# Kernel tuning notes

Measured on AMD Instinct MI355X. Metric: run time of the kernel, lower is better.

## Reference

```python
import jax, jax.numpy as jnp
import numpy as np

SEQ = 2048
HIDDEN = 2048
INPUT = 2048
THETA = 3
TRUNC = 128  # truncated-BPTT length (divides SEQ)


def setup_inputs() -> dict:
    key = jax.random.key(0)
    k0, k1, k2, k3, k4 = jax.random.split(key, 5)
    inp = jax.random.normal(k0, (1, SEQ, INPUT), jnp.float32)
    internal = jax.random.normal(k1, (THETA + 1, SEQ, HIDDEN), jnp.float32) * 0.1
    state = jax.random.normal(k2, (1, 1, HIDDEN), jnp.float32) * 0.1
    weight_ih = jax.random.normal(k3, (HIDDEN, INPUT), jnp.float32) / np.sqrt(INPUT).astype(np.float32)
    weight_hh = jax.random.normal(k4, (HIDDEN, HIDDEN), jnp.float32) * np.float32(0.5 / np.sqrt(HIDDEN))
    bias = jnp.zeros((HIDDEN,), jnp.float32)
    return {"input": inp, "internal": internal, "state": state,
            "weight_ih": weight_ih, "weight_hh": weight_hh, "bias": bias,
            "theta": THETA}


def reference(input, internal, state, weight_ih, weight_hh, bias, theta):
    theta = int(theta)
    seq = input.shape[1]
    hidden = weight_hh.shape[0]
    # pad input along theta dim to theta+1 (torch: F.pad with zeros at the end of dim 0)
    x = jnp.pad(input, ((0, theta + 1 - input.shape[0]), (0, 0), (0, 0)))
    # Precompute the input-driven part of the cell for every (theta, t):
    # cell: h' = relu(x @ Wih^T + internal + bias + h @ Whh^T)
    pre = jnp.einsum('tsi,hi->tsh', x, weight_ih) + internal + bias  # [theta+1, seq, hidden]
    n_chunks = seq // TRUNC
    # [n_chunks, TRUNC, theta+1, hidden]
    pre_c = pre.transpose(1, 0, 2).reshape(n_chunks, TRUNC, theta + 1, hidden)

    def cell(p, h):
        return jax.nn.relu(p + h @ weight_hh.T)

    def step(h, pre_t):  # pre_t: [theta+1, hidden]
        h0 = cell(pre_t[0], h)
        outs = [h0]
        hth = h0
        for th in range(1, theta + 1):
            hth = cell(pre_t[th], hth)
            outs.append(hth)
        # continuousTheta=False: carry state from the base (th=0) step
        return h0, jnp.stack(outs, 0)  # [theta+1, hidden]

    def chunk(h, pre_chunk):
        h, outs = jax.lax.scan(step, h, pre_chunk)
        # truncated BPTT: detach state between chunks (identity in fwd)
        return jax.lax.stop_gradient(h), outs

    h0 = state[0, 0]  # [hidden]
    h_final, outs = jax.lax.scan(chunk, h0, pre_c)
    # outs: [n_chunks, TRUNC, theta+1, hidden] -> [theta+1, seq, hidden]
    outputs = outs.reshape(seq, theta + 1, hidden).transpose(1, 0, 2)
    return outputs, h_final[None, None, :]
```

## Files before the change

### kernel.cpp

```cpp
#include <hip/hip_runtime.h>
#include <stdint.h>

#define SEQ 2048
#define HID 2048
#define INP 2048
#define NTH 4

typedef uint32_t u32x4 __attribute__((ext_vector_type(4)));

template<int CTRL>
__device__ __forceinline__ float dpp_add(float x) {
    int y = __builtin_amdgcn_update_dpp(0, __float_as_int(x), CTRL, 0xF, 0xF, true);
    return x + __int_as_float(y);
}
__device__ __forceinline__ float wave_sum64(float x) {
    x = dpp_add<0x111>(x);
    x = dpp_add<0x112>(x);
    x = dpp_add<0x114>(x);
    x = dpp_add<0x118>(x);
    x = dpp_add<0x142>(x);
    x = dpp_add<0x143>(x);
    return x;
}

template<int RELU>
__global__ __launch_bounds__(256, 2)
void gemm_abt(const float* __restrict__ A, const float* __restrict__ B,
              const float* __restrict__ D, const float* __restrict__ bias,
              float* __restrict__ C, int M, int N, int K) {
    __shared__ float sA[16][132];
    __shared__ float sB[16][68];
    const int tid = threadIdx.x;
    const int tx  = tid & 15;
    const int ty  = tid >> 4;
    const int m0  = blockIdx.y * 128;
    const int n0  = blockIdx.x * 64;

    float acc[8][4];
#pragma unroll
    for (int i = 0; i < 8; ++i)
#pragma unroll
        for (int j = 0; j < 4; ++j) acc[i][j] = 0.f;

    const int srow = tid >> 2;
    const int skq  = (tid & 3) * 4;

    for (int kt = 0; kt < K; kt += 16) {
#pragma unroll
        for (int s = 0; s < 2; ++s) {
            const int row = srow + s * 64;
            float4 va = *reinterpret_cast<const float4*>(&A[(size_t)(m0 + row) * K + kt + skq]);
            sA[skq + 0][row] = va.x; sA[skq + 1][row] = va.y;
            sA[skq + 2][row] = va.z; sA[skq + 3][row] = va.w;
        }
        {
            float4 vb = *reinterpret_cast<const float4*>(&B[(size_t)(n0 + srow) * K + kt + skq]);
            sB[skq + 0][srow] = vb.x; sB[skq + 1][srow] = vb.y;
            sB[skq + 2][srow] = vb.z; sB[skq + 3][srow] = vb.w;
        }
        __syncthreads();
#pragma unroll
        for (int k = 0; k < 16; ++k) {
            float a[8], b[4];
            *reinterpret_cast<float4*>(&a[0]) = *reinterpret_cast<const float4*>(&sA[k][ty * 8]);
            *reinterpret_cast<float4*>(&a[4]) = *reinterpret_cast<const float4*>(&sA[k][ty * 8 + 4]);
            *reinterpret_cast<float4*>(&b[0]) = *reinterpret_cast<const float4*>(&sB[k][tx * 4]);
#pragma unroll
            for (int i = 0; i < 8; ++i)
#pragma unroll
                for (int j = 0; j < 4; ++j)
                    acc[i][j] = fmaf(a[i], b[j], acc[i][j]);
        }
        __syncthreads();
    }

#pragma unroll
    for (int i = 0; i < 8; ++i) {
        const size_t m = (size_t)(m0 + ty * 8 + i);
        const size_t n = (size_t)(n0 + tx * 4);
        float4 d  = *reinterpret_cast<const float4*>(&D[m * N + n]);
        float4 bz = *reinterpret_cast<const float4*>(&bias[n]);
        float4 o;
        o.x = acc[i][0] + d.x + bz.x;
        o.y = acc[i][1] + d.y + bz.y;
        o.z = acc[i][2] + d.z + bz.z;
        o.w = acc[i][3] + d.w + bz.w;
        if (RELU) {
            o.x = fmaxf(o.x, 0.f); o.y = fmaxf(o.y, 0.f);
            o.z = fmaxf(o.z, 0.f); o.w = fmaxf(o.w, 0.f);
        }
        *reinterpret_cast<float4*>(&C[m * N + n]) = o;
    }
}

__global__ void init_state_k(const float* __restrict__ state,
                             unsigned long long* __restrict__ slots) {
    const int i = blockIdx.x * 256 + threadIdx.x;
    slots[i] = (unsigned long long)__float_as_uint(state[i]);
}

__global__ __launch_bounds__(1024, 1)
void rnn_scan(const float* __restrict__ Whh, float* __restrict__ out0,
              unsigned long long* __restrict__ slots, float* __restrict__ tail) {
    __shared__ float hl[HID];
    __shared__ float part[2][32];
    const int tid  = threadIdx.x;
    const int lane = tid & 63;
    const int wv   = tid >> 6;
    const int half = wv >> 3;
    const int g    = wv & 7;
    const int base = blockIdx.x * 32;
    const int kb   = half * 1024 + lane * 4;

    float4 wrow[4][4];
#pragma unroll
    for (int rr = 0; rr < 4; ++rr)
#pragma unroll
        for (int j = 0; j < 4; ++j)
            wrow[rr][j] = *reinterpret_cast<const float4*>(
                &Whh[(size_t)(base + g * 4 + rr) * HID + kb + j * 256]);

    for (int t = 0; t < SEQ; ++t) {
        float pre = 0.f;
        if (tid < 32) pre = out0[(size_t)t * HID + base + tid];

        const unsigned long long* sp =
            slots + (size_t)(t & 3) * HID + (size_t)tid * 2;
        const uint32_t tag = (uint32_t)t;
        u32x4 q;
        for (;;) {
            asm volatile(
                "global_load_dwordx4 %0, %1, off sc0 sc1\n\t"
                "s_waitcnt vmcnt(0)"
                : "=&v"(q)
                : "v"(sp)
                : "memory");
            if (q.y == tag && q.w == tag) break;
            __builtin_amdgcn_s_sleep(1);
        }
        hl[tid * 2 + 0] = __uint_as_float(q.x);
        hl[tid * 2 + 1] = __uint_as_float(q.z);
        __syncthreads();

        float acc0 = 0.f, acc1 = 0.f, acc2 = 0.f, acc3 = 0.f;
#pragma unroll
        for (int j = 0; j < 4; ++j) {
            const float4 hv = *reinterpret_cast<const float4*>(&hl[kb + j * 256]);
            acc0 = fmaf(wrow[0][j].x, hv.x, acc0); acc0 = fmaf(wrow[0][j].y, hv.y, acc0);
            acc0 = fmaf(wrow[0][j].z, hv.z, acc0); acc0 = fmaf(wrow[0][j].w, hv.w, acc0);
            acc1 = fmaf(wrow[1][j].x, hv.x, acc1); acc1 = fmaf(wrow[1][j].y, hv.y, acc1);
            acc1 = fmaf(wrow[1][j].z, hv.z, acc1); acc1 = fmaf(wrow[1][j].w, hv.w, acc1);
            acc2 = fmaf(wrow[2][j].x, hv.x, acc2); acc2 = fmaf(wrow[2][j].y, hv.y, acc2);
            acc2 = fmaf(wrow[2][j].z, hv.z, acc2); acc2 = fmaf(wrow[2][j].w, hv.w, acc2);
            acc3 = fmaf(wrow[3][j].x, hv.x, acc3); acc3 = fmaf(wrow[3][j].y, hv.y, acc3);
            acc3 = fmaf(wrow[3][j].z, hv.z, acc3); acc3 = fmaf(wrow[3][j].w, hv.w, acc3);
        }
        acc0 = wave_sum64(acc0);
        acc1 = wave_sum64(acc1);
        acc2 = wave_sum64(acc2);
        acc3 = wave_sum64(acc3);
        if (lane == 63)
            *reinterpret_cast<float4*>(&part[half][g * 4]) =
                make_float4(acc0, acc1, acc2, acc3);
        __syncthreads();

        if (tid < 32) {
            const int grow = base + tid;
            const float h = fmaxf(part[0][tid] + part[1][tid] + pre, 0.f);
            out0[(size_t)t * HID + grow] = h;
            const unsigned long long pk =
                ((unsigned long long)(uint32_t)(t + 1) << 32) | __float_as_uint(h);
            __hip_atomic_store(&slots[(size_t)((t + 1) & 3) * HID + grow], pk,
                               __ATOMIC_RELAXED, __HIP_MEMORY_SCOPE_AGENT);
            if (t == SEQ - 1) tail[grow] = h;
        }
    }
}

extern "C" void kernel_launch(void* const* d_in, const int* in_sizes, int n_in,
                              void* d_out, int out_size, void* d_ws, size_t ws_size,
                              hipStream_t stream) {
    const float* input    = (const float*)d_in[0];
    const float* internal = (const float*)d_in[1];
    const float* state    = (const float*)d_in[2];
    const float* wih      = (const float*)d_in[3];
    const float* whh      = (const float*)d_in[4];
    const float* bias     = (const float*)d_in[5];

    float* out = (float*)d_out;
    unsigned long long* slots = (unsigned long long*)d_ws;
    const size_t SH = (size_t)SEQ * HID;

    gemm_abt<0><<<dim3(HID / 64, SEQ / 128), 256, 0, stream>>>(
        input, wih, internal, bias, out, SEQ, HID, INP);
    init_state_k<<<8, 256, 0, stream>>>(state, slots);
    rnn_scan<<<64, 1024, 0, stream>>>(whh, out, slots, out + (size_t)NTH * SH);
    for (int th = 1; th < NTH; ++th)
        gemm_abt<1><<<dim3(HID / 64, SEQ / 128), 256, 0, stream>>>(
            out + (size_t)(th - 1) * SH, whh, internal + (size_t)th * SH, bias,
            out + (size_t)th * SH, SEQ, HID, HID);
}
```

Baseline: 4.582 ms.

## Replace fp32 SIMT GEMMs with split-bf16 (3-term) MFMA GEMMs

Adds a conversion kernel that splits each fp32 operand into bf16 hi/lo parts, interleaved so that a K dimension three times longer computes hi*hi + hi*lo + lo*hi. The four large GEMMs then run on bf16 MFMA instructions with direct global-to-LDS loads and a swizzled shared-memory layout. This moves the dense matmul work off the fp32 FMA path and onto matrix cores while keeping roughly fp32-level accuracy. The cost is three times as many MMA operations, extra conversion passes over the activations between theta steps, and a large workspace buffer. The old path is kept as a fallback when the workspace is too small.

```diff
diff --git a/kernel.cpp b/kernel.cpp
--- a/kernel.cpp
+++ b/kernel.cpp
@@ -5,8 +5,12 @@
 #define HID 2048
 #define INP 2048
 #define NTH 4
-
-typedef uint32_t u32x4 __attribute__((ext_vector_type(4)));
+#define K3  (HID*3)
+
+typedef uint32_t u32x4  __attribute__((ext_vector_type(4)));
+typedef short    short8 __attribute__((ext_vector_type(8)));
+typedef float    f32x4  __attribute__((ext_vector_type(4)));
+typedef uint32_t uint4v __attribute__((ext_vector_type(4)));
 
 template<int CTRL>
 __device__ __forceinline__ float dpp_add(float x) {
@@ -14,13 +18,117 @@
     return x + __int_as_float(y);
 }
 __device__ __forceinline__ float wave_sum64(float x) {
-    x = dpp_add<0x111>(x);
-    x = dpp_add<0x112>(x);
-    x = dpp_add<0x114>(x);
-    x = dpp_add<0x118>(x);
-    x = dpp_add<0x142>(x);
-    x = dpp_add<0x143>(x);
+    x = dpp_add<0x111>(x); x = dpp_add<0x112>(x); x = dpp_add<0x114>(x);
+    x = dpp_add<0x118>(x); x = dpp_add<0x142>(x); x = dpp_add<0x143>(x);
     return x;
+}
+
+__device__ __forceinline__ ushort bf16h(float x) {
+    uint32_t u = __float_as_uint(x);
+    return (ushort)((u + 0x7fffu + ((u >> 16) & 1u)) >> 16);
+}
+template<int BSIDE>
+__global__ __launch_bounds__(256)
+void convert3_k(const float* __restrict__ X, ushort* __restrict__ X3) {
+    const size_t t = (size_t)blockIdx.x * 256 + threadIdx.x;
+    float xs[8];
+    *reinterpret_cast<float4*>(&xs[0]) = *reinterpret_cast<const float4*>(X + t * 8);
+    *reinterpret_cast<float4*>(&xs[4]) = *reinterpret_cast<const float4*>(X + t * 8 + 4);
+    ushort o[24];
+#pragma unroll
+    for (int i = 0; i < 8; ++i) {
+        const ushort hi = bf16h(xs[i]);
+        const float hif = __uint_as_float(((uint32_t)hi) << 16);
+        const ushort lo = bf16h(xs[i] - hif);
+        o[i * 3 + 0] = hi;
+        o[i * 3 + 1] = BSIDE ? lo : hi;
+        o[i * 3 + 2] = BSIDE ? hi : lo;
+    }
+    ushort* pd = X3 + t * 24;
+#pragma unroll
+    for (int v = 0; v < 3; ++v)
+        *reinterpret_cast<uint4v*>(pd + v * 8) = *reinterpret_cast<const uint4v*>(&o[v * 8]);
+}
+
+template<int RELU>
+__global__ __launch_bounds__(256, 2)
+void mfma_gemm(const ushort* __restrict__ A3, const ushort* __restrict__ B3,
+               const float* __restrict__ D, const float* __restrict__ bias,
+               float* __restrict__ C) {
+    __shared__ ushort sA[128 * 64];
+    __shared__ ushort sB[64 * 64];
+    const int tid = threadIdx.x;
+    const int w = tid >> 6, lane = tid & 63;
+    const int m0 = blockIdx.y * 128, n0 = blockIdx.x * 64;
+
+    f32x4 acc[2][4];
+#pragma unroll
+    for (int m = 0; m < 2; ++m)
+#pragma unroll
+        for (int n = 0; n < 4; ++n) acc[m][n] = (f32x4)0.f;
+
+    const int c16s = (lane & 7) ^ ((lane >> 3) & 7);
+
+    for (int kt = 0; kt < K3; kt += 64) {
+#pragma unroll
+        for (int i = 0; i < 4; ++i) {
+            const int c = w * 4 + i;
+            const int row = c * 8 + (lane >> 3);
+            const ushort* src = A3 + (size_t)(m0 + row) * K3 + kt + c16s * 8;
+            __builtin_amdgcn_global_load_lds(
+                (const __attribute__((address_space(1))) uint32_t*)src,
+                (__attribute__((address_space(3))) uint32_t*)(sA + c * 512), 16, 0, 0);
+        }
+#pragma unroll
+        for (int i = 0; i < 2; ++i) {
+            const int c = w * 2 + i;
+            const int row = c * 8 + (lane >> 3);
+            const ushort* src = B3 + (size_t)(n0 + row) * K3 + kt + c16s * 8;
+            __builtin_amdgcn_global_load_lds(
+                (const __attribute__((address_space(1))) uint32_t*)src,
+                (__attribute__((address_space(3))) uint32_t*)(sB + c * 512), 16, 0, 0);
+        }
+        __syncthreads();
+
+#pragma unroll
+        for (int ks = 0; ks < 2; ++ks) {
+            short8 af[2], bf[4];
+#pragma unroll
+            for (int m = 0; m < 2; ++m) {
+                const int row = w * 32 + m * 16 + (lane & 15);
+                const int c16 = (ks * 4 + (lane >> 4)) ^ (row & 7);
+                af[m] = *reinterpret_cast<const short8*>(sA + row * 64 + c16 * 8);
+            }
+#pragma unroll
+            for (int n = 0; n < 4; ++n) {
+                const int row = n * 16 + (lane & 15);
+                const int c16 = (ks * 4 + (lane >> 4)) ^ (row & 7);
+                bf[n] = *reinterpret_cast<const short8*>(sB + row * 64 + c16 * 8);
+            }
+#pragma unroll
+            for (int m = 0; m < 2; ++m)
+#pragma unroll
+                for (int n = 0; n < 4; ++n)
+                    acc[m][n] = __builtin_amdgcn_mfma_f32_16x16x32_bf16(
+                        af[m], bf[n], acc[m][n], 0, 0, 0);
+        }
+        __syncthreads();
+    }
+
+#pragma unroll
+    for (int m = 0; m < 2; ++m)
+#pragma unroll
+        for (int n = 0; n < 4; ++n) {
+            const int col = n0 + n * 16 + (lane & 15);
+            const float bz = bias[col];
+#pragma unroll
+            for (int r = 0; r < 4; ++r) {
+                const int rowm = m0 + w * 32 + m * 16 + (lane >> 4) * 4 + r;
+                float v = acc[m][n][r] + D[(size_t)rowm * HID + col] + bz;
+                if (RELU) v = fmaxf(v, 0.f);
+                C[(size_t)rowm * HID + col] = v;
+            }
+        }
 }
 
 template<int RELU>
@@ -31,20 +139,14 @@
     __shared__ float sA[16][132];
     __shared__ float sB[16][68];
     const int tid = threadIdx.x;
-    const int tx  = tid & 15;
-    const int ty  = tid >> 4;
-    const int m0  = blockIdx.y * 128;
-    const int n0  = blockIdx.x * 64;
-
+    const int tx = tid & 15, ty = tid >> 4;
+    const int m0 = blockIdx.y * 128, n0 = blockIdx.x * 64;
     float acc[8][4];
 #pragma unroll
     for (int i = 0; i < 8; ++i)
 #pragma unroll
         for (int j = 0; j < 4; ++j) acc[i][j] = 0.f;
-
-    const int srow = tid >> 2;
-    const int skq  = (tid & 3) * 4;
-
+    const int srow = tid >> 2, skq = (tid & 3) * 4;
     for (int kt = 0; kt < K; kt += 16) {
 #pragma unroll
         for (int s = 0; s < 2; ++s) {
@@ -68,23 +170,19 @@
 #pragma unroll
             for (int i = 0; i < 8; ++i)
 #pragma unroll
-                for (int j = 0; j < 4; ++j)
-                    acc[i][j] = fmaf(a[i], b[j], acc[i][j]);
-        }
-        __syncthreads();
-    }
-
+                for (int j = 0; j < 4; ++j) acc[i][j] = fmaf(a[i], b[j], acc[i][j]);
+        }
+        __syncthreads();
+    }
 #pragma unroll
     for (int i = 0; i < 8; ++i) {
         const size_t m = (size_t)(m0 + ty * 8 + i);
         const size_t n = (size_t)(n0 + tx * 4);
-        float4 d  = *reinterpret_cast<const float4*>(&D[m * N + n]);
+        float4 d = *reinterpret_cast<const float4*>(&D[m * N + n]);
         float4 bz = *reinterpret_cast<const float4*>(&bias[n]);
         float4 o;
-        o.x = acc[i][0] + d.x + bz.x;
-        o.y = acc[i][1] + d.y + bz.y;
-        o.z = acc[i][2] + d.z + bz.z;
-        o.w = acc[i][3] + d.w + bz.w;
+        o.x = acc[i][0] + d.x + bz.x; o.y = acc[i][1] + d.y + bz.y;
+        o.z = acc[i][2] + d.z + bz.z; o.w = acc[i][3] + d.w + bz.w;
         if (RELU) {
             o.x = fmaxf(o.x, 0.f); o.y = fmaxf(o.y, 0.f);
             o.z = fmaxf(o.z, 0.f); o.w = fmaxf(o.w, 0.f);
@@ -132,9 +230,7 @@
             asm volatile(
                 "global_load_dwordx4 %0, %1, off sc0 sc1\n\t"
                 "s_waitcnt vmcnt(0)"
-                : "=&v"(q)
-                : "v"(sp)
-                : "memory");
+                : "=&v"(q) : "v"(sp) : "memory");
             if (q.y == tag && q.w == tag) break;
             __builtin_amdgcn_s_sleep(1);
         }
@@ -155,10 +251,8 @@
             acc3 = fmaf(wrow[3][j].x, hv.x, acc3); acc3 = fmaf(wrow[3][j].y, hv.y, acc3);
             acc3 = fmaf(wrow[3][j].z, hv.z, acc3); acc3 = fmaf(wrow[3][j].w, hv.w, acc3);
         }
-        acc0 = wave_sum64(acc0);
-        acc1 = wave_sum64(acc1);
-        acc2 = wave_sum64(acc2);
-        acc3 = wave_sum64(acc3);
+        acc0 = wave_sum64(acc0); acc1 = wave_sum64(acc1);
+        acc2 = wave_sum64(acc2); acc3 = wave_sum64(acc3);
         if (lane == 63)
             *reinterpret_cast<float4*>(&part[half][g * 4]) =
                 make_float4(acc0, acc1, acc2, acc3);
@@ -190,13 +284,35 @@
     float* out = (float*)d_out;
     unsigned long long* slots = (unsigned long long*)d_ws;
     const size_t SH = (size_t)SEQ * HID;
-
-    gemm_abt<0><<<dim3(HID / 64, SEQ / 128), 256, 0, stream>>>(
-        input, wih, internal, bias, out, SEQ, HID, INP);
-    init_state_k<<<8, 256, 0, stream>>>(state, slots);
-    rnn_scan<<<64, 1024, 0, stream>>>(whh, out, slots, out + (size_t)NTH * SH);
-    for (int th = 1; th < NTH; ++th)
-        gemm_abt<1><<<dim3(HID / 64, SEQ / 128), 256, 0, stream>>>(
-            out + (size_t)(th - 1) * SH, whh, internal + (size_t)th * SH, bias,
-            out + (size_t)th * SH, SEQ, HID, HID);
-}
+    const size_t CVT = (size_t)HID * K3 * sizeof(ushort);
+    const size_t need = 65536 + 3 * CVT;
+
+    const dim3 cgrid((HID * INP / 8) / 256);
+    if (ws_size >= need) {
+        ushort* B3whh = (ushort*)((char*)d_ws + 65536);
+        ushort* B3wih = (ushort*)((char*)d_ws + 65536 + CVT);
+        ushort* A3    = (ushort*)((char*)d_ws + 65536 + 2 * CVT);
+
+        convert3_k<1><<<cgrid, 256, 0, stream>>>(wih, B3wih);
+        convert3_k<0><<<cgrid, 256, 0, stream>>>(input, A3);
+        mfma_gemm<0><<<dim3(HID / 64, SEQ / 128), 256, 0, stream>>>(
+            A3, B3wih, internal, bias, out);
+        convert3_k<1><<<cgrid, 256, 0, stream>>>(whh, B3whh);
+        init_state_k<<<8, 256, 0, stream>>>(state, slots);
+        rnn_scan<<<64, 1024, 0, stream>>>(whh, out, slots, out + (size_t)NTH * SH);
+        for (int th = 1; th < NTH; ++th) {
+            convert3_k<0><<<cgrid, 256, 0, stream>>>(out + (size_t)(th - 1) * SH, A3);
+            mfma_gemm<1><<<dim3(HID / 64, SEQ / 128), 256, 0, stream>>>(
+                A3, B3whh, internal + (size_t)th * SH, bias, out + (size_t)th * SH);
+        }
+    } else {
+        gemm_abt<0><<<dim3(HID / 64, SEQ / 128), 256, 0, stream>>>(
+            input, wih, internal, bias, out, SEQ, HID, INP);
+        init_state_k<<<8, 256, 0, stream>>>(state, slots);
+        rnn_scan<<<64, 1024, 0, stream>>>(whh, out, slots, out + (size_t)NTH * SH);
+        for (int th = 1; th < NTH; ++th)
+            gemm_abt<1><<<dim3(HID / 64, SEQ / 128), 256, 0, stream>>>(
+                out + (size_t)(th - 1) * SH, whh, internal + (size_t)th * SH, bias,
+                out + (size_t)th * SH, SEQ, HID, HID);
+    }
+}
```

Measured after the change: 3.884 ms. 1.18x faster.
